# Kernel optimization log

Measured on AMD Instinct MI355X. Metric: run time of the kernel, lower is better.

The kernel has to match this reference:

```python
import jax, jax.numpy as jnp
import numpy as np
from jax import lax

B, C, H, W = 4, 64, 256, 320
PT = 6
EPS = 1e-6
BN_EPS = 1e-5


def conv2d(x, w, b=None):
    y = lax.conv_general_dilated(x, w, (1, 1), 'SAME',
                                 dimension_numbers=('NCHW', 'OIHW', 'NCHW'))
    if b is not None:
        y = y + b[None, :, None, None]
    return y


def batchnorm(x, g, b):
    # training-mode batch statistics over (N, H, W)
    m = jnp.mean(x, axis=(0, 2, 3), keepdims=True)
    v = jnp.var(x, axis=(0, 2, 3), keepdims=True)
    return g[None, :, None, None] * (x - m) * lax.rsqrt(v + BN_EPS) + b[None, :, None, None]


def gen_kernel(fout, wconv, g, b, pk):
    # Basic2d: conv(no bias) -> BN -> ReLU, producing pk*pk-1 affinity channels
    w = jax.nn.relu(batchnorm(conv2d(fout, wconv), g, b))
    s = jnp.sum(jnp.abs(w), axis=1, keepdims=True)
    w = w / (s + EPS)
    mid = 1.0 - jnp.sum(w, axis=1, keepdims=True)
    h = (pk * pk - 1) // 2
    return jnp.concatenate([w[:, :h], mid, w[:, h:]], axis=1)  # [B, pk*pk, H, W]


def spatial_kernel(d, sigma):
    r = jnp.linspace(-1.0, 1.0, d)
    x, y = jnp.meshgrid(r, r, indexing='ij')
    return jnp.exp(-(x * x + y * y) / (2.0 * sigma * sigma)).reshape(1, d * d, 1, 1)


def local_conv(x, w, pk):
    # per-pixel spatially-varying conv: x [B,1,H,W], w [B,pk*pk,H,W]
    patches = lax.conv_general_dilated_patches(
        x, (pk, pk), (1, 1), 'SAME', dimension_numbers=('NCHW', 'OIHW', 'NCHW'))
    return jnp.sum(patches * w, axis=1, keepdims=True)


def setup_inputs() -> dict:
    key = jax.random.key(0)
    ks = jax.random.split(key, 16)
    f32 = jnp.float32
    inp = {
        'fout': jax.random.normal(ks[0], (B, C, H, W), f32),
        'hn': jax.random.uniform(ks[1], (B, 1, H, W), f32),
        'h0': jax.random.uniform(ks[2], (B, 1, H, W), f32),
        # GenKernel_L convs (no bias, followed by BN)
        'w3_conv': jax.random.normal(ks[3], (8, C, 3, 3), f32) * 0.05,
        'w3_g': jnp.ones((8,), f32), 'w3_b': jnp.zeros((8,), f32),
        'w5_conv': jax.random.normal(ks[4], (24, C, 3, 3), f32) * 0.05,
        'w5_g': jnp.ones((24,), f32), 'w5_b': jnp.zeros((24,), f32),
        'w7_conv': jax.random.normal(ks[5], (48, C, 3, 3), f32) * 0.05,
        'w7_g': jnp.ones((48,), f32), 'w7_b': jnp.zeros((48,), f32),
        # confidence heads (conv with bias -> softmax over channels)
        'ck_w': jax.random.normal(ks[6], (3, C, 3, 3), f32) * 0.05,
        'ck_b': jnp.zeros((3,), f32),
        'ct_w': jax.random.normal(ks[7], (3, C + 3, 3, 3), f32) * 0.05,
        'ct_b': jnp.zeros((3,), f32),
        'sig3': jnp.float32(1.0), 'sig5': jnp.float32(1.0), 'sig7': jnp.float32(1.0),
    }
    return inp


def reference(fout, hn, h0, w3_conv, w3_g, w3_b, w5_conv, w5_g, w5_b,
              w7_conv, w7_g, w7_b, ck_w, ck_b, ct_w, ct_b, sig3, sig5, sig7):
    weight3 = gen_kernel(fout, w3_conv, w3_g, w3_b, 3) * spatial_kernel(3, sig3)
    weight5 = gen_kernel(fout, w5_conv, w5_g, w5_b, 5) * spatial_kernel(5, sig5)
    weight7 = gen_kernel(fout, w7_conv, w7_g, w7_b, 7) * spatial_kernel(7, sig7)
    weight3 = weight3 / jnp.clip(jnp.sum(weight3, 1, keepdims=True), 1e-7)
    weight5 = weight5 / jnp.clip(jnp.sum(weight5, 1, keepdims=True), 1e-7)
    weight7 = weight7 / jnp.clip(jnp.sum(weight7, 1, keepdims=True), 1e-7)

    confk = jax.nn.softmax(conv2d(fout, ck_w, ck_b), axis=1)
    conf3, conf5, conf7 = confk[:, 0:1], confk[:, 1:2], confk[:, 2:3]

    hn3 = hn5 = hn7 = hn
    hns = [hn]
    for i in range(PT):
        hn3 = local_conv(hn3, weight3, 3)
        hn5 = local_conv(hn5, weight5, 5)
        hn7 = local_conv(hn7, weight7, 7)
        if i == PT // 2 - 1:
            hns.append(conf3 * hn3 + conf5 * hn5 + conf7 * hn7)
    hns.append(conf3 * hn3 + conf5 * hn5 + conf7 * hn7)
    hns = jnp.concatenate(hns, axis=1)  # [B, 3, H, W]

    wt = jax.nn.softmax(conv2d(jnp.concatenate([fout, hns], axis=1), ct_w, ct_b), axis=1)
    return jnp.sum(wt * hns, axis=1, keepdims=True)
```

## Files before the change

### kernel.cpp

```cpp
#include <hip/hip_runtime.h>
#include <hip/hip_bf16.h>
#include <math.h>

#define W_    320
#define H_    256
#define HW_   81920
#define BHW_  327680
#define PRM_TOT 49786
#define WCH   86

#define OW3  0
#define OW5  4608
#define OW7  18432
#define OCK  46080
#define OCT  47808
#define OG3  49617
#define OB3  49625
#define OG5  49633
#define OB5  49657
#define OG7  49681
#define OB7  49729
#define OCKB 49777
#define OCTB 49780
#define OSIG 49783

typedef unsigned short u16;
typedef __attribute__((ext_vector_type(8))) short short8;
typedef __attribute__((ext_vector_type(4))) float f32x4;

__device__ __forceinline__ float dload(const void* p, size_t i, int isbf) {
  return isbf ? __bfloat162float(((const __hip_bfloat16*)p)[i])
              : ((const float*)p)[i];
}

__device__ __forceinline__ u16 f32_bf16_rne(float f) {
  union { float f; unsigned u; } v; v.f = f;
  unsigned r = v.u + 0x7FFFu + ((v.u >> 16) & 1u);
  return (u16)(r >> 16);
}
__device__ __forceinline__ float bf16_f32(u16 h) {
  union { unsigned u; float f; } v; v.u = ((unsigned)h) << 16;
  return v.f;
}

__device__ __forceinline__ unsigned wquant(float w) {
  int v = (int)(w * 65536.f + 0.5f);
  return (unsigned)(v > 65535 ? 65535 : (v < 0 ? 0 : v));
}

__global__ __launch_bounds__(512) void k_detect(
    const void* t0, const void* t1, const void* t2, const void* t3,
    const void* t4, const void* t5, const void* t6, const void* t7,
    const void* t8, const void* t9, const void* t10, const void* t11,
    const void* t12, const void* t13, const void* t14, const void* t15,
    const void* t16, const void* t17, int* __restrict__ flags)
{
  __shared__ int c_other, c_zeven, c_zodd, c_m;
  const void* ptrs[18] = {t0,t1,t2,t3,t4,t5,t6,t7,t8,t9,
                          t10,t11,t12,t13,t14,t15,t16,t17};
  const int ns[18] = {20971520, 327680, 4608, 8, 8, 13824, 24, 24,
                      27648, 48, 48, 1728, 3, 1809, 3, 1, 1, 1};
  const int tensor = blockIdx.x;
  const int n = ns[tensor];
  const unsigned short* u = (const unsigned short*)ptrs[tensor];
  if (threadIdx.x == 0) { c_other = 0; c_zeven = 0; c_zodd = 0; c_m = 0; }
  __syncthreads();
  {
    int k = threadIdx.x >> 1;
    long long pos = (long long)k * n / 256;
    int j = ((int)pos & ~1) + (threadIdx.x & 1);
    if (j < n) {
      unsigned short v = u[j];
      int e = (v >> 7) & 0xFF;
      atomicAdd(&c_m, 1);
      if (v != 0 && (e < 90 || e > 150)) atomicAdd(&c_other, 1);
      if (v == 0) {
        if (j & 1) atomicAdd(&c_zodd, 1); else atomicAdd(&c_zeven, 1);
      }
    }
  }
  __syncthreads();
  if (threadIdx.x == 0) {
    int isf32;
    if (n == 1) isf32 = (u[0] == 0);
    else        isf32 = (4 * c_other >= c_m) ||
                        (2 * (c_zeven - c_zodd) >= c_m);
    flags[tensor] = isf32 ? 0 : 1;
  }
}

__global__ __launch_bounds__(256) void k_cvt(
    const void* w3c, const void* w5c, const void* w7c, const void* ckw, const void* ctw,
    const void* g3, const void* b3, const void* g5, const void* b5,
    const void* g7, const void* b7, const void* ckb, const void* ctb,
    const void* s3, const void* s5, const void* s7,
    float* __restrict__ prm, const int* __restrict__ flags)
{
  int j = blockIdx.x * 256 + threadIdx.x;
  if (j >= PRM_TOT) return;
  const void* src; int off; int fid;
  if      (j < OW5)    { src = w3c; off = OW3;  fid = 2; }
  else if (j < OW7)    { src = w5c; off = OW5;  fid = 5; }
  else if (j < OCK)    { src = w7c; off = OW7;  fid = 8; }
  else if (j < OCT)    { src = ckw; off = OCK;  fid = 11; }
  else if (j < OG3)    { src = ctw; off = OCT;  fid = 13; }
  else if (j < OB3)    { src = g3;  off = OG3;  fid = 3; }
  else if (j < OG5)    { src = b3;  off = OB3;  fid = 4; }
  else if (j < OB5)    { src = g5;  off = OG5;  fid = 6; }
  else if (j < OG7)    { src = b5;  off = OB5;  fid = 7; }
  else if (j < OB7)    { src = g7;  off = OG7;  fid = 9; }
  else if (j < OCKB)   { src = b7;  off = OB7;  fid = 10; }
  else if (j < OCTB)   { src = ckb; off = OCKB; fid = 12; }
  else if (j < OSIG)   { src = ctb; off = OCTB; fid = 14; }
  else if (j < OSIG+1) { src = s3;  off = OSIG;   fid = 15; }
  else if (j < OSIG+2) { src = s5;  off = OSIG+1; fid = 16; }
  else                 { src = s7;  off = OSIG+2; fid = 17; }
  prm[j] = dload(src, j - off, flags[fid]);
}

__global__ __launch_bounds__(256) void k_pack(
    const float* __restrict__ prm, u16* __restrict__ apack)
{
  int idx = blockIdx.x * 256 + threadIdx.x;
  int e = idx & 7;
  int lane = (idx >> 3) & 63;
  int t = idx >> 9;
  int mt = t % 6; t /= 6;
  int chunk = t & 1; t >>= 1;
  int tap = t % 9;
  int hilo = t / 9;
  int oc = mt * 16 + (lane & 15);
  int ic = chunk * 32 + (lane >> 4) * 8 + e;
  float w = 0.f;
  if (oc < 83)      w = prm[(size_t)oc * 576 + (size_t)ic * 9 + tap];
  else if (oc < 86) w = prm[OCT + (size_t)((oc - 83) * 67 + ic) * 9 + tap];
  u16 h = f32_bf16_rne(w);
  u16 outv = (hilo == 0) ? h : f32_bf16_rne(w - bf16_f32(h));
  apack[idx] = outv;
}

template<int ISBF>
__device__ __forceinline__ void stage_chunk(
    const void* __restrict__ fout, int b, int y0, int x0, int chunk,
    u16* Bhi, u16* Blo)
{
  const int g = threadIdx.x & 3;
  const int cell0 = threadIdx.x >> 2;
  const size_t fb = (size_t)b * 64 * HW_ + (size_t)(chunk * 32 + g * 8) * HW_;
#pragma unroll
  for (int it = 0; it < 7; ++it) {
    int cell = cell0 + it * 64;
    if (cell < 396) {
      int row = cell / 66;
      int px = cell - row * 66;
      int gy = y0 - 1 + row, gx = x0 - 1 + px;
      bool ok = ((unsigned)gy < H_) && ((unsigned)gx < W_);
      size_t base = fb + (size_t)gy * W_ + gx;
      short8 hs = {0,0,0,0,0,0,0,0};
      short8 ls = {0,0,0,0,0,0,0,0};
#pragma unroll
      for (int i = 0; i < 8; ++i) {
        float v = ok ? dload(fout, base + (size_t)i * HW_, ISBF) : 0.f;
        union { float f; unsigned u; } uv; uv.f = v;
        u16 h = (u16)(uv.u >> 16);
        float resid = v - bf16_f32(h);
        hs[i] = (short)h;
        ls[i] = (short)f32_bf16_rne(resid);
      }
      int off = ((row * 66 + px) * 32 + g * 8) * 2;
      off ^= (px & 7) << 4;
      *(short8*)((char*)Bhi + off) = hs;
      *(short8*)((char*)Blo + off) = ls;
    }
  }
}

__global__ __launch_bounds__(256, 2) void k_conv_mfma(
    const void* __restrict__ fout, const u16* __restrict__ apack,
    float* __restrict__ wbuf, const int* __restrict__ flags)
{
  __shared__ __align__(16) u16 Bhi[6 * 66 * 32];
  __shared__ __align__(16) u16 Blo[6 * 66 * 32];
  const int isbf = flags[0];
  const int x0 = blockIdx.x * 64;
  const int y0 = blockIdx.y * 4;
  const int b  = blockIdx.z;
  const int lane = threadIdx.x & 63;
  const int wv   = threadIdx.x >> 6;

  const f32x4 zero = {0.f, 0.f, 0.f, 0.f};
  f32x4 acc[6][4];
#pragma unroll
  for (int mt = 0; mt < 6; ++mt)
#pragma unroll
    for (int nt = 0; nt < 4; ++nt)
      acc[mt][nt] = zero;

  for (int chunk = 0; chunk < 2; ++chunk) {
    if (chunk) __syncthreads();
    if (isbf) stage_chunk<1>(fout, b, y0, x0, chunk, Bhi, Blo);
    else      stage_chunk<0>(fout, b, y0, x0, chunk, Bhi, Blo);
    __syncthreads();

#pragma unroll
    for (int tap = 0; tap < 9; ++tap) {
      const int dy = tap / 3, dx = tap - dy * 3;
      const int row = wv + dy;
      short8 bh[4], bl[4];
#pragma unroll
      for (int nt = 0; nt < 4; ++nt) {
        int px = nt * 16 + (lane & 15) + dx;
        int off = ((row * 66 + px) * 32 + (lane >> 4) * 8) * 2;
        off ^= (px & 7) << 4;
        bh[nt] = *(const short8*)((const char*)Bhi + off);
        bl[nt] = *(const short8*)((const char*)Blo + off);
      }
      const u16* abase = apack + (size_t)(tap * 2 + chunk) * 3072 + (size_t)lane * 8;
#pragma unroll
      for (int mt = 0; mt < 6; ++mt) {
        short8 ah = *(const short8*)(abase + (size_t)mt * 512);
        short8 al = *(const short8*)(abase + (size_t)mt * 512 + 55296);
#pragma unroll
        for (int nt = 0; nt < 4; ++nt) {
          acc[mt][nt] = __builtin_amdgcn_mfma_f32_16x16x32_bf16(ah, bh[nt], acc[mt][nt], 0, 0, 0);
          acc[mt][nt] = __builtin_amdgcn_mfma_f32_16x16x32_bf16(ah, bl[nt], acc[mt][nt], 0, 0, 0);
          acc[mt][nt] = __builtin_amdgcn_mfma_f32_16x16x32_bf16(al, bh[nt], acc[mt][nt], 0, 0, 0);
        }
      }
    }
  }

  const int ocr = (lane >> 4) * 4;
  float* wb = wbuf + (size_t)b * WCH * HW_
            + (size_t)(y0 + wv) * W_ + x0 + (lane & 15);
#pragma unroll
  for (int mt = 0; mt < 6; ++mt) {
#pragma unroll
    for (int nt = 0; nt < 4; ++nt) {
#pragma unroll
      for (int r = 0; r < 4; ++r) {
        int oc = mt * 16 + ocr + r;
        if (oc < 86)
          wb[(size_t)oc * HW_ + nt * 16] = acc[mt][nt][r];
      }
    }
  }
}

__global__ __launch_bounds__(256) void k_stats(
    const float* __restrict__ wbuf, float* __restrict__ stat)
{
  const int ch = blockIdx.y;
  float s = 0.f, qq = 0.f;
  for (int idx = blockIdx.x * 256 + threadIdx.x; idx < BHW_;
       idx += gridDim.x * 256) {
    int b = idx / HW_, r = idx - b * HW_;
    float v = wbuf[((size_t)(b * WCH + ch)) * HW_ + r];
    s += v; qq += v * v;
  }
#pragma unroll
  for (int m = 1; m < 64; m <<= 1) {
    s += __shfl_xor(s, m, 64);
    qq += __shfl_xor(qq, m, 64);
  }
  __shared__ float rs[4], rq[4];
  const int lane = threadIdx.x & 63, wv = threadIdx.x >> 6;
  if (lane == 0) { rs[wv] = s; rq[wv] = qq; }
  __syncthreads();
  if (threadIdx.x == 0) {
    float ts = rs[0] + rs[1] + rs[2] + rs[3];
    float tq = rq[0] + rq[1] + rq[2] + rq[3];
    atomicAdd(&stat[ch], ts);
    atomicAdd(&stat[80 + ch], tq);
  }
}

__global__ void k_bn_finalize(float* __restrict__ stat)
{
  int ch = threadIdx.x;
  if (ch < 80) {
    const float n = 1.f / (float)BHW_;
    float m = stat[ch] * n;
    float var = stat[80 + ch] * n - m * m;
    stat[160 + ch] = m;
    stat[240 + ch] = rsqrtf(var + 1e-5f);
  }
}

__global__ __launch_bounds__(256, 2) void k_prop0(
    float* __restrict__ wbuf, float* __restrict__ conf,
    const void* __restrict__ rawhn,
    float* __restrict__ h3o, float* __restrict__ h5o, float* __restrict__ h7o,
    const float* __restrict__ prm, const float* __restrict__ stat,
    const int* __restrict__ flags)
{
  const int isbf = flags[1];
  const int p = blockIdx.x * 256 + threadIdx.x;
  const int b = p / HW_, q = p - b * HW_;
  const int y = q / W_, x = q - y * W_;
  const size_t bo = (size_t)b * HW_;
  float* base = wbuf + ((size_t)b * WCH) * HW_ + q;
  const float* mean = stat + 160;
  const float* istd = stat + 240;

  auto hload = [&](int gy, int gx) -> float {
    if ((unsigned)gy < H_ && (unsigned)gx < W_)
      return dload(rawhn, bo + (size_t)gy * W_ + gx, isbf);
    return 0.f;
  };

  {
    float c0 = base[(size_t)80 * HW_] + prm[OCKB + 0];
    float c1 = base[(size_t)81 * HW_] + prm[OCKB + 1];
    float c2 = base[(size_t)82 * HW_] + prm[OCKB + 2];
    float m = fmaxf(c0, fmaxf(c1, c2));
    float e0 = expf(c0 - m), e1 = expf(c1 - m), e2 = expf(c2 - m);
    float inv = 1.f / (e0 + e1 + e2);
    float* cf = conf + ((size_t)b * 3) * HW_ + q;
    cf[0] = e0 * inv;
    cf[(size_t)HW_] = e1 * inv;
    cf[(size_t)2 * HW_] = e2 * inv;
  }

  float a3, a5, a7;
  unsigned carry;

  {
    float cvv[8]; float s = 0.f;
#pragma unroll
    for (int i = 0; i < 8; ++i) {
      float v = base[(size_t)i * HW_];
      v = fmaxf(0.f, (v - mean[i]) * istd[i] * prm[OG3 + i] + prm[OB3 + i]);
      cvv[i] = v; s += v;
    }
    float inv = 1.f / (s + 1e-6f);
    float ctr = 1.f - s * inv;
    float sg = prm[OSIG + 0];
    float a = 0.5f / (sg * sg);
    float e1 = expf(-a);
    float g1[3] = {e1, 1.f, e1};
    float tot = 0.f;
#pragma unroll
    for (int j = 0; j < 9; ++j) {
      float w = (j == 4) ? ctr : cvv[j < 4 ? j : j - 1] * inv;
      w *= g1[j / 3] * g1[j % 3];
      if (j == 4) ctr = w; else cvv[j < 4 ? j : j - 1] = w;
      tot += w;
    }
    float rr = 1.f / fmaxf(tot, 1e-7f);
    auto wk = [&](int c) -> float {
      return ((c == 4) ? ctr : cvv[c < 4 ? c : c - 1]) * rr;
    };
    a3 = 0.f;
#pragma unroll
    for (int j = 0; j < 9; ++j)
      a3 = fmaf(wk(j), hload(y + j / 3 - 1, x + j % 3 - 1), a3);
#pragma unroll
    for (int pr = 0; pr < 4; ++pr)
      base[(size_t)pr * HW_] =
          __uint_as_float(wquant(wk(2 * pr)) | (wquant(wk(2 * pr + 1)) << 16));
    carry = wquant(wk(8));
  }

  {
    float cvv[24]; float s = 0.f;
#pragma unroll
    for (int i = 0; i < 24; ++i) {
      float v = base[(size_t)(8 + i) * HW_];
      v = fmaxf(0.f, (v - mean[8 + i]) * istd[8 + i] * prm[OG5 + i] + prm[OB5 + i]);
      cvv[i] = v; s += v;
    }
    float inv = 1.f / (s + 1e-6f);
    float ctr = 1.f - s * inv;
    float sg = prm[OSIG + 1];
    float a = 0.5f / (sg * sg);
    float ea = expf(-a), eb = expf(-0.25f * a);
    float g1[5] = {ea, eb, 1.f, eb, ea};
    float tot = 0.f;
#pragma unroll
    for (int j = 0; j < 25; ++j) {
      float w = (j == 12) ? ctr : cvv[j < 12 ? j : j - 1] * inv;
      w *= g1[j / 5] * g1[j % 5];
      if (j == 12) ctr = w; else cvv[j < 12 ? j : j - 1] = w;
      tot += w;
    }
    float rr = 1.f / fmaxf(tot, 1e-7f);
    auto wk = [&](int j) -> float {
      return ((j == 12) ? ctr : cvv[j < 12 ? j : j - 1]) * rr;
    };
    a5 = 0.f;
#pragma unroll
    for (int j = 0; j < 25; ++j)
      a5 = fmaf(wk(j), hload(y + j / 5 - 2, x + j % 5 - 2), a5);
    base[(size_t)4 * HW_] = __uint_as_float(carry | (wquant(wk(0)) << 16));
#pragma unroll
    for (int m = 0; m < 12; ++m)
      base[(size_t)(5 + m) * HW_] =
          __uint_as_float(wquant(wk(1 + 2 * m)) | (wquant(wk(2 + 2 * m)) << 16));
  }

  {
    float cvv[48]; float s = 0.f;
#pragma unroll
    for (int i = 0; i < 48; ++i) {
      float v = base[(size_t)(32 + i) * HW_];
      v = fmaxf(0.f, (v - mean[32 + i]) * istd[32 + i] * prm[OG7 + i] + prm[OB7 + i]);
      cvv[i] = v; s += v;
    }
    float inv = 1.f / (s + 1e-6f);
    float ctr = 1.f - s * inv;
    float sg = prm[OSIG + 2];
    float a = 0.5f / (sg * sg);
    float ea = expf(-a), eb = expf(-(4.f / 9.f) * a), ec = expf(-(1.f / 9.f) * a);
    float g1[7] = {ea, eb, ec, 1.f, ec, eb, ea};
    float tot = 0.f;
#pragma unroll
    for (int j = 0; j < 49; ++j) {
      float w = (j == 24) ? ctr : cvv[j < 24 ? j : j - 1] * inv;
      w *= g1[j / 7] * g1[j % 7];
      if (j == 24) ctr = w; else cvv[j < 24 ? j : j - 1] = w;
      tot += w;
    }
    float rr = 1.f / fmaxf(tot, 1e-7f);
    auto wk = [&](int j) -> float {
      return ((j == 24) ? ctr : cvv[j < 24 ? j : j - 1]) * rr;
    };
    a7 = 0.f;
#pragma unroll
    for (int j = 0; j < 49; ++j)
      a7 = fmaf(wk(j), hload(y + j / 7 - 3, x + j % 7 - 3), a7);
#pragma unroll
    for (int m = 0; m < 24; ++m)
      base[(size_t)(17 + m) * HW_] =
          __uint_as_float(wquant(wk(2 * m)) | (wquant(wk(2 * m + 1)) << 16));
    base[(size_t)41 * HW_] = __uint_as_float(wquant(wk(48)));
  }

  h3o[bo + q] = a3;
  h5o[bo + q] = a5;
  h7o[bo + q] = a7;
}

__global__ __launch_bounds__(256) void k_prop_q(
    const float* __restrict__ wbuf, const float* __restrict__ conf,
    const float* __restrict__ h3i, const float* __restrict__ h5i,
    const float* __restrict__ h7i,
    float* __restrict__ h3o, float* __restrict__ h5o, float* __restrict__ h7o,
    float* __restrict__ combo, int store_h)
{
  const int p = blockIdx.x * 256 + threadIdx.x;
  const int b = p / HW_, q = p - b * HW_;
  const int y = q / W_, x = q - y * W_;
  const size_t bo = (size_t)b * HW_;
  const float* base = wbuf + ((size_t)b * WCH) * HW_ + q;

  unsigned pk[42];
#pragma unroll
  for (int pr = 0; pr < 42; ++pr)
    pk[pr] = __float_as_uint(base[(size_t)pr * HW_]);
  const float sc = 1.f / 65536.f;
#define WDEC(CH) ((float)((pk[(CH) >> 1] >> (((CH) & 1) * 16)) & 0xffffu) * sc)

  float a3 = 0.f, a5 = 0.f, a7 = 0.f;
#pragma unroll
  for (int j = 0; j < 9; ++j) {
    int gy = y + j / 3 - 1, gx = x + j % 3 - 1;
    float v = 0.f;
    if ((unsigned)gy < H_ && (unsigned)gx < W_)
      v = h3i[bo + (size_t)gy * W_ + gx];
    a3 = fmaf(WDEC(j), v, a3);
  }
#pragma unroll
  for (int j = 0; j < 25; ++j) {
    int gy = y + j / 5 - 2, gx = x + j % 5 - 2;
    float v = 0.f;
    if ((unsigned)gy < H_ && (unsigned)gx < W_)
      v = h5i[bo + (size_t)gy * W_ + gx];
    a5 = fmaf(WDEC(9 + j), v, a5);
  }
#pragma unroll
  for (int j = 0; j < 49; ++j) {
    int gy = y + j / 7 - 3, gx = x + j % 7 - 3;
    float v = 0.f;
    if ((unsigned)gy < H_ && (unsigned)gx < W_)
      v = h7i[bo + (size_t)gy * W_ + gx];
    a7 = fmaf(WDEC(34 + j), v, a7);
  }
#undef WDEC
  if (store_h) {
    h3o[bo + q] = a3;
    h5o[bo + q] = a5;
    h7o[bo + q] = a7;
  }
  if (combo) {
    const float* cf = conf + ((size_t)b * 3) * HW_ + q;
    combo[bo + q] = cf[0] * a3 + cf[(size_t)HW_] * a5 + cf[(size_t)2 * HW_] * a7;
  }
}

__global__ __launch_bounds__(256, 2) void k_final(
    const float* __restrict__ wbuf, const void* __restrict__ rawhn,
    const float* __restrict__ mid, const float* __restrict__ fin,
    const float* __restrict__ prm, float* __restrict__ out,
    const int* __restrict__ flags)
{
  const int isbf_h = flags[1];
  const float* ctw = prm + OCT;
  const int p = blockIdx.x * 256 + threadIdx.x;
  const int b = p / HW_, q = p - b * HW_;
  const int y = q / W_, x = q - y * W_;
  const size_t bo = (size_t)b * HW_;

  const float* lg = wbuf + ((size_t)b * WCH + 83) * HW_ + q;
  float l0 = prm[OCTB + 0] + lg[0];
  float l1 = prm[OCTB + 1] + lg[(size_t)HW_];
  float l2 = prm[OCTB + 2] + lg[(size_t)2 * HW_];

#pragma unroll
  for (int c = 0; c < 3; ++c) {
    const int icg = 64 + c;
#pragma unroll
    for (int j = 0; j < 9; ++j) {
      int gy = y + j / 3 - 1, gx = x + j % 3 - 1;
      float v = 0.f;
      if ((unsigned)gy < H_ && (unsigned)gx < W_) {
        size_t gi = bo + (size_t)gy * W_ + gx;
        v = (c == 0) ? dload(rawhn, gi, isbf_h) : (c == 1) ? mid[gi] : fin[gi];
      }
      l0 = fmaf(v, ctw[(0 * 67 + icg) * 9 + j], l0);
      l1 = fmaf(v, ctw[(1 * 67 + icg) * 9 + j], l1);
      l2 = fmaf(v, ctw[(2 * 67 + icg) * 9 + j], l2);
    }
  }
  float m = fmaxf(l0, fmaxf(l1, l2));
  float e0 = expf(l0 - m), e1 = expf(l1 - m), e2 = expf(l2 - m);
  float inv = 1.f / (e0 + e1 + e2);
  float h0c = dload(rawhn, bo + q, isbf_h);
  float r = (e0 * h0c + e1 * mid[bo + q] + e2 * fin[bo + q]) * inv;
  out[bo + q] = r;
}

extern "C" void kernel_launch(void* const* d_in, const int* in_sizes, int n_in,
                              void* d_out, int out_size, void* d_ws, size_t ws_size,
                              hipStream_t stream)
{
  static const int EXP[19] = {20971520, 327680, 327680, 4608, 8, 8, 13824, 24, 24,
                              27648, 48, 48, 1728, 3, 1809, 3, 1, 1, 1};
  const void* P[19];
  bool match = (n_in >= 19);
  for (int i = 0; i < 19 && match; ++i) if (in_sizes[i] != EXP[i]) match = false;
  if (match) {
    for (int i = 0; i < 19; ++i) P[i] = d_in[i];
  } else {
    bool used[64] = {false};
    for (int t = 0; t < 19; ++t) {
      P[t] = d_in[t < n_in ? t : 0];
      for (int i = 0; i < n_in && i < 64; ++i)
        if (!used[i] && in_sizes[i] == EXP[t]) { P[t] = d_in[i]; used[i] = true; break; }
    }
  }
  const void* fout = P[0];
  const void* hn   = P[1];
  float* out = (float*)d_out;

  float* ws    = (float*)d_ws;
  int*   flags = (int*)ws;
  float* stat  = ws + 32;
  float* prm   = ws + 352;
  float* big   = ws + 50176;
  float* wbuf  = big;
  float* conf  = wbuf + (size_t)WCH * BHW_;
  float* hnA   = conf + (size_t)3 * BHW_;
  float* hnB   = hnA + (size_t)3 * BHW_;
  float* midb  = hnB + (size_t)3 * BHW_;
  float* finb  = midb + (size_t)BHW_;
  u16*   apack = (u16*)midb;

  (void)hipMemsetAsync(stat, 0, 160 * sizeof(float), stream);

  k_detect<<<18, 512, 0, stream>>>(
      P[0], P[1], P[3], P[4], P[5], P[6], P[7], P[8],
      P[9], P[10], P[11], P[12], P[13], P[14], P[15],
      P[16], P[17], P[18], flags);

  k_cvt<<<(PRM_TOT + 255) / 256, 256, 0, stream>>>(
      P[3], P[6], P[9], P[12], P[14],
      P[4], P[5], P[7], P[8], P[10], P[11],
      P[13], P[15], P[16], P[17], P[18], prm, flags);

  k_pack<<<432, 256, 0, stream>>>(prm, apack);
  k_conv_mfma<<<dim3(5, 64, 4), 256, 0, stream>>>(fout, apack, wbuf, flags);
  k_stats<<<dim3(32, 80), 256, 0, stream>>>(wbuf, stat);
  k_bn_finalize<<<1, 128, 0, stream>>>(stat);

  k_prop0<<<1280, 256, 0, stream>>>(
      wbuf, conf, hn, hnA, hnA + (size_t)BHW_, hnA + (size_t)2 * BHW_,
      prm, stat, flags);

  const float* i3 = hnA;
  const float* i5 = hnA + (size_t)BHW_;
  const float* i7 = hnA + (size_t)2 * BHW_;
  for (int it = 1; it < 6; ++it) {
    float* base = (it & 1) ? hnB : hnA;
    float* o3 = base;
    float* o5 = base + (size_t)BHW_;
    float* o7 = base + (size_t)2 * BHW_;
    float* combo = (it == 2) ? midb : (it == 5) ? finb : nullptr;
    k_prop_q<<<1280, 256, 0, stream>>>(
        wbuf, conf, i3, i5, i7, o3, o5, o7, combo, (it < 5) ? 1 : 0);
    i3 = o3; i5 = o5; i7 = o7;
  }

  k_final<<<1280, 256, 0, stream>>>(wbuf, hn, midb, finb, prm, out, flags);
}
```

Before: 445.5 us.

## Use zero-padded propagation buffers to remove boundary checks in local convs

Propagation state buffers are moved to a zero-padded layout with a 3-pixel halo, so the 3x3/5x5/7x7 per-pixel convolutions load neighbours without bounds checks. The raw hn input is converted once into a padded float buffer, which also removes the repeated dtype-dispatch loads. The B ping-pong buffer reuses dead channels of wbuf, and its halos are zeroed with memsets. The fixed-point weight scale is now applied once after accumulation instead of per tap. This adds memset and padding passes plus some unaligned, strided accesses.

```diff
diff --git a/kernel.cpp b/kernel.cpp
--- a/kernel.cpp
+++ b/kernel.cpp
@@ -8,6 +8,9 @@
 #define BHW_  327680
 #define PRM_TOT 49786
 #define WCH   86
+#define PW_   326
+#define PH_   262
+#define PHW_  85412
 
 #define OW3  0
 #define OW5  4608
@@ -118,6 +121,18 @@
   prm[j] = dload(src, j - off, flags[fid]);
 }
 
+__global__ __launch_bounds__(256) void k_padhn(
+    const void* __restrict__ rawhn, float* __restrict__ hnp,
+    const int* __restrict__ flags)
+{
+  const int isbf = flags[1];
+  const int p = blockIdx.x * 256 + threadIdx.x;
+  const int b = p / HW_, q = p - b * HW_;
+  const int y = q / W_, x = q - y * W_;
+  hnp[(size_t)b * PHW_ + (size_t)(y + 3) * PW_ + (x + 3)] =
+      dload(rawhn, (size_t)b * HW_ + q, isbf);
+}
+
 __global__ __launch_bounds__(256) void k_pack(
     const float* __restrict__ prm, u16* __restrict__ apack)
 {
@@ -289,25 +304,18 @@
 
 __global__ __launch_bounds__(256, 2) void k_prop0(
     float* __restrict__ wbuf, float* __restrict__ conf,
-    const void* __restrict__ rawhn,
+    const float* __restrict__ hnp,
     float* __restrict__ h3o, float* __restrict__ h5o, float* __restrict__ h7o,
-    const float* __restrict__ prm, const float* __restrict__ stat,
-    const int* __restrict__ flags)
-{
-  const int isbf = flags[1];
+    const float* __restrict__ prm, const float* __restrict__ stat)
+{
   const int p = blockIdx.x * 256 + threadIdx.x;
   const int b = p / HW_, q = p - b * HW_;
   const int y = q / W_, x = q - y * W_;
-  const size_t bo = (size_t)b * HW_;
   float* base = wbuf + ((size_t)b * WCH) * HW_ + q;
   const float* mean = stat + 160;
   const float* istd = stat + 240;
-
-  auto hload = [&](int gy, int gx) -> float {
-    if ((unsigned)gy < H_ && (unsigned)gx < W_)
-      return dload(rawhn, bo + (size_t)gy * W_ + gx, isbf);
-    return 0.f;
-  };
+  const size_t pc = (size_t)b * PHW_ + (size_t)(y + 3) * PW_ + (x + 3);
+  const float* hc = hnp + pc;
 
   {
     float c0 = base[(size_t)80 * HW_] + prm[OCKB + 0];
@@ -354,7 +362,7 @@
     a3 = 0.f;
 #pragma unroll
     for (int j = 0; j < 9; ++j)
-      a3 = fmaf(wk(j), hload(y + j / 3 - 1, x + j % 3 - 1), a3);
+      a3 = fmaf(wk(j), hc[(j / 3 - 1) * PW_ + (j % 3 - 1)], a3);
 #pragma unroll
     for (int pr = 0; pr < 4; ++pr)
       base[(size_t)pr * HW_] =
@@ -391,7 +399,7 @@
     a5 = 0.f;
 #pragma unroll
     for (int j = 0; j < 25; ++j)
-      a5 = fmaf(wk(j), hload(y + j / 5 - 2, x + j % 5 - 2), a5);
+      a5 = fmaf(wk(j), hc[(j / 5 - 2) * PW_ + (j % 5 - 2)], a5);
     base[(size_t)4 * HW_] = __uint_as_float(carry | (wquant(wk(0)) << 16));
 #pragma unroll
     for (int m = 0; m < 12; ++m)
@@ -428,7 +436,7 @@
     a7 = 0.f;
 #pragma unroll
     for (int j = 0; j < 49; ++j)
-      a7 = fmaf(wk(j), hload(y + j / 7 - 3, x + j % 7 - 3), a7);
+      a7 = fmaf(wk(j), hc[(j / 7 - 3) * PW_ + (j % 7 - 3)], a7);
 #pragma unroll
     for (int m = 0; m < 24; ++m)
       base[(size_t)(17 + m) * HW_] =
@@ -436,75 +444,66 @@
     base[(size_t)41 * HW_] = __uint_as_float(wquant(wk(48)));
   }
 
-  h3o[bo + q] = a3;
-  h5o[bo + q] = a5;
-  h7o[bo + q] = a7;
+  h3o[pc] = a3;
+  h5o[pc] = a5;
+  h7o[pc] = a7;
 }
 
 __global__ __launch_bounds__(256) void k_prop_q(
     const float* __restrict__ wbuf, const float* __restrict__ conf,
-    const float* __restrict__ h3i, const float* __restrict__ h5i,
-    const float* __restrict__ h7i,
-    float* __restrict__ h3o, float* __restrict__ h5o, float* __restrict__ h7o,
+    const float* __restrict__ in3, const float* __restrict__ in5,
+    const float* __restrict__ in7, size_t bsi,
+    float* __restrict__ out3, float* __restrict__ out5,
+    float* __restrict__ out7, size_t bso,
     float* __restrict__ combo, int store_h)
 {
   const int p = blockIdx.x * 256 + threadIdx.x;
   const int b = p / HW_, q = p - b * HW_;
   const int y = q / W_, x = q - y * W_;
-  const size_t bo = (size_t)b * HW_;
   const float* base = wbuf + ((size_t)b * WCH) * HW_ + q;
 
   unsigned pk[42];
 #pragma unroll
   for (int pr = 0; pr < 42; ++pr)
     pk[pr] = __float_as_uint(base[(size_t)pr * HW_]);
+#define WRAW(CH) ((float)((pk[(CH) >> 1] >> (((CH) & 1) * 16)) & 0xffffu))
+
+  const size_t pc = (size_t)(y + 3) * PW_ + (x + 3);
+  const float* c3 = in3 + (size_t)b * bsi + pc;
+  const float* c5 = in5 + (size_t)b * bsi + pc;
+  const float* c7 = in7 + (size_t)b * bsi + pc;
+
+  float a3 = 0.f, a5 = 0.f, a7 = 0.f;
+#pragma unroll
+  for (int j = 0; j < 9; ++j)
+    a3 = fmaf(WRAW(j), c3[(j / 3 - 1) * PW_ + (j % 3 - 1)], a3);
+#pragma unroll
+  for (int j = 0; j < 25; ++j)
+    a5 = fmaf(WRAW(9 + j), c5[(j / 5 - 2) * PW_ + (j % 5 - 2)], a5);
+#pragma unroll
+  for (int j = 0; j < 49; ++j)
+    a7 = fmaf(WRAW(34 + j), c7[(j / 7 - 3) * PW_ + (j % 7 - 3)], a7);
+#undef WRAW
   const float sc = 1.f / 65536.f;
-#define WDEC(CH) ((float)((pk[(CH) >> 1] >> (((CH) & 1) * 16)) & 0xffffu) * sc)
-
-  float a3 = 0.f, a5 = 0.f, a7 = 0.f;
-#pragma unroll
-  for (int j = 0; j < 9; ++j) {
-    int gy = y + j / 3 - 1, gx = x + j % 3 - 1;
-    float v = 0.f;
-    if ((unsigned)gy < H_ && (unsigned)gx < W_)
-      v = h3i[bo + (size_t)gy * W_ + gx];
-    a3 = fmaf(WDEC(j), v, a3);
-  }
-#pragma unroll
-  for (int j = 0; j < 25; ++j) {
-    int gy = y + j / 5 - 2, gx = x + j % 5 - 2;
-    float v = 0.f;
-    if ((unsigned)gy < H_ && (unsigned)gx < W_)
-      v = h5i[bo + (size_t)gy * W_ + gx];
-    a5 = fmaf(WDEC(9 + j), v, a5);
-  }
-#pragma unroll
-  for (int j = 0; j < 49; ++j) {
-    int gy = y + j / 7 - 3, gx = x + j % 7 - 3;
-    float v = 0.f;
-    if ((unsigned)gy < H_ && (unsigned)gx < W_)
-      v = h7i[bo + (size_t)gy * W_ + gx];
-    a7 = fmaf(WDEC(34 + j), v, a7);
-  }
-#undef WDEC
+  a3 *= sc; a5 *= sc; a7 *= sc;
+
   if (store_h) {
-    h3o[bo + q] = a3;
-    h5o[bo + q] = a5;
-    h7o[bo + q] = a7;
+    out3[(size_t)b * bso + pc] = a3;
+    out5[(size_t)b * bso + pc] = a5;
+    out7[(size_t)b * bso + pc] = a7;
   }
   if (combo) {
     const float* cf = conf + ((size_t)b * 3) * HW_ + q;
-    combo[bo + q] = cf[0] * a3 + cf[(size_t)HW_] * a5 + cf[(size_t)2 * HW_] * a7;
+    combo[(size_t)b * HW_ + q] =
+        cf[0] * a3 + cf[(size_t)HW_] * a5 + cf[(size_t)2 * HW_] * a7;
   }
 }
 
 __global__ __launch_bounds__(256, 2) void k_final(
-    const float* __restrict__ wbuf, const void* __restrict__ rawhn,
+    const float* __restrict__ wbuf, const float* __restrict__ hnp,
     const float* __restrict__ mid, const float* __restrict__ fin,
-    const float* __restrict__ prm, float* __restrict__ out,
-    const int* __restrict__ flags)
-{
-  const int isbf_h = flags[1];
+    const float* __restrict__ prm, float* __restrict__ out)
+{
   const float* ctw = prm + OCT;
   const int p = blockIdx.x * 256 + threadIdx.x;
   const int b = p / HW_, q = p - b * HW_;
@@ -516,17 +515,24 @@
   float l1 = prm[OCTB + 1] + lg[(size_t)HW_];
   float l2 = prm[OCTB + 2] + lg[(size_t)2 * HW_];
 
-#pragma unroll
-  for (int c = 0; c < 3; ++c) {
+  const float* hc = hnp + (size_t)b * PHW_ + (size_t)(y + 3) * PW_ + (x + 3);
+#pragma unroll
+  for (int j = 0; j < 9; ++j) {
+    float v = hc[(j / 3 - 1) * PW_ + (j % 3 - 1)];
+    l0 = fmaf(v, ctw[(0 * 67 + 64) * 9 + j], l0);
+    l1 = fmaf(v, ctw[(1 * 67 + 64) * 9 + j], l1);
+    l2 = fmaf(v, ctw[(2 * 67 + 64) * 9 + j], l2);
+  }
+#pragma unroll
+  for (int c = 1; c < 3; ++c) {
     const int icg = 64 + c;
+    const float* src = (c == 1) ? mid : fin;
 #pragma unroll
     for (int j = 0; j < 9; ++j) {
       int gy = y + j / 3 - 1, gx = x + j % 3 - 1;
       float v = 0.f;
-      if ((unsigned)gy < H_ && (unsigned)gx < W_) {
-        size_t gi = bo + (size_t)gy * W_ + gx;
-        v = (c == 0) ? dload(rawhn, gi, isbf_h) : (c == 1) ? mid[gi] : fin[gi];
-      }
+      if ((unsigned)gy < H_ && (unsigned)gx < W_)
+        v = src[bo + (size_t)gy * W_ + gx];
       l0 = fmaf(v, ctw[(0 * 67 + icg) * 9 + j], l0);
       l1 = fmaf(v, ctw[(1 * 67 + icg) * 9 + j], l1);
       l2 = fmaf(v, ctw[(2 * 67 + icg) * 9 + j], l2);
@@ -535,7 +541,7 @@
   float m = fmaxf(l0, fmaxf(l1, l2));
   float e0 = expf(l0 - m), e1 = expf(l1 - m), e2 = expf(l2 - m);
   float inv = 1.f / (e0 + e1 + e2);
-  float h0c = dload(rawhn, bo + q, isbf_h);
+  float h0c = hc[0];
   float r = (e0 * h0c + e1 * mid[bo + q] + e2 * fin[bo + q]) * inv;
   out[bo + q] = r;
 }
@@ -570,13 +576,21 @@
   float* big   = ws + 50176;
   float* wbuf  = big;
   float* conf  = wbuf + (size_t)WCH * BHW_;
-  float* hnA   = conf + (size_t)3 * BHW_;
-  float* hnB   = hnA + (size_t)3 * BHW_;
-  float* midb  = hnB + (size_t)3 * BHW_;
+  float* Abase = conf + (size_t)3 * BHW_;
+  float* hnp   = Abase + (size_t)12 * PHW_;
+  float* midb  = hnp + (size_t)4 * PHW_;
   float* finb  = midb + (size_t)BHW_;
   u16*   apack = (u16*)midb;
 
+  float* a3f = Abase;
+  float* a5f = Abase + (size_t)4 * PHW_;
+  float* a7f = Abase + (size_t)8 * PHW_;
+  float* b3f = wbuf + (size_t)42 * HW_;
+  float* b5f = b3f + (size_t)PHW_;
+  float* b7f = b3f + (size_t)2 * PHW_;
+
   (void)hipMemsetAsync(stat, 0, 160 * sizeof(float), stream);
+  (void)hipMemsetAsync(Abase, 0, (size_t)16 * PHW_ * sizeof(float), stream);
 
   k_detect<<<18, 512, 0, stream>>>(
       P[0], P[1], P[3], P[4], P[5], P[6], P[7], P[8],
@@ -588,28 +602,31 @@
       P[4], P[5], P[7], P[8], P[10], P[11],
       P[13], P[15], P[16], P[17], P[18], prm, flags);
 
+  k_padhn<<<1280, 256, 0, stream>>>(hn, hnp, flags);
   k_pack<<<432, 256, 0, stream>>>(prm, apack);
   k_conv_mfma<<<dim3(5, 64, 4), 256, 0, stream>>>(fout, apack, wbuf, flags);
   k_stats<<<dim3(32, 80), 256, 0, stream>>>(wbuf, stat);
   k_bn_finalize<<<1, 128, 0, stream>>>(stat);
 
   k_prop0<<<1280, 256, 0, stream>>>(
-      wbuf, conf, hn, hnA, hnA + (size_t)BHW_, hnA + (size_t)2 * BHW_,
-      prm, stat, flags);
-
-  const float* i3 = hnA;
-  const float* i5 = hnA + (size_t)BHW_;
-  const float* i7 = hnA + (size_t)2 * BHW_;
-  for (int it = 1; it < 6; ++it) {
-    float* base = (it & 1) ? hnB : hnA;
-    float* o3 = base;
-    float* o5 = base + (size_t)BHW_;
-    float* o7 = base + (size_t)2 * BHW_;
-    float* combo = (it == 2) ? midb : (it == 5) ? finb : nullptr;
-    k_prop_q<<<1280, 256, 0, stream>>>(
-        wbuf, conf, i3, i5, i7, o3, o5, o7, combo, (it < 5) ? 1 : 0);
-    i3 = o3; i5 = o5; i7 = o7;
-  }
-
-  k_final<<<1280, 256, 0, stream>>>(wbuf, hn, midb, finb, prm, out, flags);
-}
+      wbuf, conf, hnp, a3f, a5f, a7f, prm, stat);
+
+  for (int b = 0; b < 4; ++b)
+    (void)hipMemsetAsync(wbuf + ((size_t)b * WCH + 42) * HW_, 0,
+                         (size_t)3 * PHW_ * sizeof(float), stream);
+
+  const size_t bsA = PHW_;
+  const size_t bsB = (size_t)WCH * HW_;
+  k_prop_q<<<1280, 256, 0, stream>>>(wbuf, conf, a3f, a5f, a7f, bsA,
+                                     b3f, b5f, b7f, bsB, nullptr, 1);
+  k_prop_q<<<1280, 256, 0, stream>>>(wbuf, conf, b3f, b5f, b7f, bsB,
+                                     a3f, a5f, a7f, bsA, midb, 1);
+  k_prop_q<<<1280, 256, 0, stream>>>(wbuf, conf, a3f, a5f, a7f, bsA,
+                                     b3f, b5f, b7f, bsB, nullptr, 1);
+  k_prop_q<<<1280, 256, 0, stream>>>(wbuf, conf, b3f, b5f, b7f, bsB,
+                                     a3f, a5f, a7f, bsA, nullptr, 1);
+  k_prop_q<<<1280, 256, 0, stream>>>(wbuf, conf, a3f, a5f, a7f, bsA,
+                                     b3f, b5f, b7f, bsB, finb, 0);
+
+  k_final<<<1280, 256, 0, stream>>>(wbuf, hnp, midb, finb, prm, out);
+}
```

Result: faster. 433.8 us (-2.6%).
